# Performance work log

Measured on AMD Instinct MI355X. Metric: run time of the kernel, lower is better.

Reference implementation:

```python
import jax, jax.numpy as jnp
import numpy as np

B, CIN, H, W = 16, 15, 256, 256
C, L, M = 64, 4, 16
ENV, D1D = 40, 4
HEAD_IN = C + ENV + D1D
BN_EPS = 1e-5


def setup_inputs() -> dict:
    key = jax.random.key(0)
    ks = iter(jax.random.split(key, 40))
    nrm = lambda shape: jax.random.normal(next(ks), shape, dtype=jnp.float32)
    scale = (2.0 / (C + C)) ** 0.5
    uni = lambda shape: scale * (jax.random.uniform(next(ks), shape, dtype=jnp.float32) - 0.5)
    d = {
        'grid': nrm((B, CIN, H, W)),
        'env': nrm((B, ENV)),
        'd1d': nrm((B, D1D)),
        'lift_w': nrm((C, CIN)) * 0.1, 'lift_b': nrm((C,)) * 0.01,
        'w1r': uni((L, C, C, M, M)), 'w1i': uni((L, C, C, M, M)),
        'w2r': uni((L, C, C, M, M)), 'w2i': uni((L, C, C, M, M)),
        'skip_w': nrm((L, C, C)) * 0.1, 'skip_b': nrm((L, C)) * 0.01,
        'bn_g': jnp.ones((L, C)), 'bn_b': jnp.zeros((L, C)),
        'bn_m': nrm((L, C)) * 0.01, 'bn_v': jnp.abs(nrm((L, C))) * 0.1 + 1.0,
        'proj_w': nrm((C, C)) * 0.1, 'proj_b': nrm((C,)) * 0.01,
        'dw1': nrm((128, HEAD_IN)) * 0.05, 'db1': nrm((128,)) * 0.01,
        'dw2': nrm((64, 128)) * 0.05, 'db2': nrm((64,)) * 0.01,
        'dw3': nrm((8, 64)) * 0.05, 'db3': nrm((8,)) * 0.01,
        'iw1': nrm((128, HEAD_IN)) * 0.05, 'ib1': nrm((128,)) * 0.01,
        'iw2': nrm((64, 128)) * 0.05, 'ib2': nrm((64,)) * 0.01,
        'iw3': nrm((4, 64)) * 0.05, 'ib3': nrm((4,)) * 0.01,
    }
    return d


def _spectral(x, w1, w2):
    # x: [B,C,H,W] real; w1,w2: [C,C,M,M] complex
    h, w = x.shape[-2], x.shape[-1]
    xft = jnp.fft.rfft2(x)  # [B,C,H,W//2+1] complex
    top = jnp.einsum('bixy,ioxy->boxy', xft[:, :, :M, :M], w1)
    bot = jnp.einsum('bixy,ioxy->boxy', xft[:, :, -M:, :M], w2)
    out_ft = jnp.zeros(xft.shape, dtype=xft.dtype)
    out_ft = out_ft.at[:, :, :M, :M].set(top).at[:, :, h - M:, :M].set(bot)
    return jnp.fft.irfft2(out_ft, s=(h, w))


def _conv1x1(x, w, b):
    return jnp.einsum('bchw,oc->bohw', x, w) + b[None, :, None, None]


def _gelu(x):
    return jax.nn.gelu(x, approximate=False)


def reference(grid, env, d1d, lift_w, lift_b, w1r, w1i, w2r, w2i, skip_w, skip_b,
              bn_g, bn_b, bn_m, bn_v, proj_w, proj_b,
              dw1, db1, dw2, db2, dw3, db3, iw1, ib1, iw2, ib2, iw3, ib3):
    x = _gelu(_conv1x1(grid, lift_w, lift_b))
    for l in range(L):
        residual = x
        w1 = w1r[l] + 1j * w1i[l]
        w2 = w2r[l] + 1j * w2i[l]
        y = _spectral(x, w1, w2) + _conv1x1(x, skip_w[l], skip_b[l])
        # BatchNorm2d in eval mode (running stats), dropout is identity at eval
        y = (y - bn_m[l][None, :, None, None]) * jax.lax.rsqrt(bn_v[l] + BN_EPS)[None, :, None, None]
        y = y * bn_g[l][None, :, None, None] + bn_b[l][None, :, None, None]
        x = _gelu(y) + residual
    x = _gelu(_conv1x1(x, proj_w, proj_b))
    x = x.mean(axis=(-2, -1))  # [B,C]
    x = jnp.concatenate([x, env, d1d], axis=-1)  # [B, C+44]
    h = _gelu(x @ dw1.T + db1)
    h = _gelu(h @ dw2.T + db2)
    out_dir = h @ dw3.T + db3
    g = _gelu(x @ iw1.T + ib1)
    g = _gelu(g @ iw2.T + ib2)
    out_int = g @ iw3.T + ib3
    return out_dir, out_int
```

## Files before the change

### kernel.cpp

```cpp
#include <hip/hip_runtime.h>
#include <hip/hip_bf16.h>
#include <math.h>

#define B_ 16
#define CIN_ 15
#define C_ 64
#define L_ 4

typedef __attribute__((ext_vector_type(8))) short short8;
typedef __attribute__((ext_vector_type(4))) short short4v;
typedef __attribute__((ext_vector_type(4))) float f32x4;

__device__ __forceinline__ float gelu_f(float x) {
    float z = fabsf(x) * 0.70710678118654752440f;
    float t = __builtin_amdgcn_rcpf(fmaf(0.3275911f, z, 1.0f));
    float p = t * fmaf(t, fmaf(t, fmaf(t, fmaf(t, 1.061405429f, -1.453152027f), 1.421413741f), -0.284496736f), 0.254829592f);
    float e = __expf(-z * z);
    float E = fmaf(-p, e, 1.0f);
    return 0.5f * fmaf(fabsf(x), E, x);
}

__device__ __forceinline__ unsigned short f2bf(float x) {
    __hip_bfloat16 h = __float2bfloat16(x);
    return *(unsigned short*)&h;
}
__device__ __forceinline__ float bf2f(unsigned short u) {
    __hip_bfloat16 h = *(__hip_bfloat16*)&u;
    return __bfloat162float(h);
}
__device__ __forceinline__ f32x4 mfma16(short8 a, short8 b, f32x4 c) {
    return __builtin_amdgcn_mfma_f32_16x16x32_bf16(a, b, c, 0, 0, 0);
}

#define TWO_PI_OVER_256 0.024543692606170259674f

__global__ __launch_bounds__(256) void k_prep(const float* __restrict__ skip_w,
                                              const float* __restrict__ bn_g, const float* __restrict__ bn_v,
                                              const float* __restrict__ proj_w,
                                              unsigned short* __restrict__ TfH, unsigned short* __restrict__ TfL,
                                              unsigned short* __restrict__ TiH, unsigned short* __restrict__ TiL,
                                              unsigned short* __restrict__ WH, unsigned short* __restrict__ WL,
                                              unsigned short* __restrict__ PH, unsigned short* __restrict__ PL,
                                              unsigned short* __restrict__ FcH, unsigned short* __restrict__ FcL,
                                              unsigned short* __restrict__ FsH, unsigned short* __restrict__ FsL,
                                              unsigned short* __restrict__ FnH, unsigned short* __restrict__ FnL,
                                              unsigned short* __restrict__ IcH, unsigned short* __restrict__ IcL,
                                              unsigned short* __restrict__ IsH, unsigned short* __restrict__ IsL,
                                              unsigned short* __restrict__ InH, unsigned short* __restrict__ InL) {
    int id = blockIdx.x * 256 + threadIdx.x;
    if (id < 8192) {
        int col = id >> 8, w = id & 255;
        int kk = (col < 16) ? col : (col - 16);
        float s, c;
        sincosf(TWO_PI_OVER_256 * (float)((w * kk) & 255), &s, &c);
        float v = (col < 16) ? c : -s;
        unsigned short hi = f2bf(v);
        TfH[id] = hi; TfL[id] = f2bf(v - bf2f(hi));
    } else if (id < 16384) {
        int idx = id - 8192;
        int w = idx >> 5, k = idx & 31, ky = k >> 1;
        float s, c;
        sincosf(TWO_PI_OVER_256 * (float)((w * ky) & 255), &s, &c);
        float v = (k & 1) ? -s : c;
        unsigned short hi = f2bf(v);
        TiH[idx] = hi; TiL[idx] = f2bf(v - bf2f(hi));
    } else if (id < 32768) {
        int idx = id - 16384;
        int lco = idx >> 6;
        float scl = bn_g[lco] * rsqrtf(bn_v[lco] + 1e-5f);
        float v = scl * skip_w[idx];
        unsigned short hi = f2bf(v);
        WH[idx] = hi; WL[idx] = f2bf(v - bf2f(hi));
    } else if (id < 36864) {
        int idx = id - 32768;
        float v = proj_w[idx];
        unsigned short hi = f2bf(v);
        PH[idx] = hi; PL[idx] = f2bf(v - bf2f(hi));
    } else if (id < 45056) {
        int idx = id - 36864;
        int j = idx >> 8, h = idx & 255;
        int kxu = j + ((j < 16) ? 0 : 224);
        float s, c;
        sincosf(TWO_PI_OVER_256 * (float)((h * kxu) & 255), &s, &c);
        unsigned short ch = f2bf(c);
        FcH[idx] = ch; FcL[idx] = f2bf(c - bf2f(ch));
        unsigned short sh = f2bf(s);
        unsigned short sl = f2bf(s - bf2f(sh));
        FsH[idx] = sh; FsL[idx] = sl;
        FnH[idx] = sh ^ 0x8000; FnL[idx] = sl ^ 0x8000;
    } else if (id < 53248) {
        int idx = id - 45056;
        int h = idx >> 5, j = idx & 31;
        int kxu = j + ((j < 16) ? 0 : 224);
        float s, c;
        sincosf(TWO_PI_OVER_256 * (float)((h * kxu) & 255), &s, &c);
        unsigned short ch = f2bf(c);
        IcH[idx] = ch; IcL[idx] = f2bf(c - bf2f(ch));
        unsigned short sh = f2bf(s);
        unsigned short sl = f2bf(s - bf2f(sh));
        IsH[idx] = sh; IsL[idx] = sl;
        InH[idx] = sh ^ 0x8000; InL[idx] = sl ^ 0x8000;
    }
}

__global__ __launch_bounds__(256) void k_lift(const float* __restrict__ g, const float* __restrict__ lw,
                                              const float* __restrict__ lb, unsigned short* __restrict__ X,
                                              const unsigned short* __restrict__ TfH, const unsigned short* __restrict__ TfL,
                                              float2* __restrict__ Y) {
    __shared__ float gs[CIN_][256];
    __shared__ float lws[C_ * CIN_];
    __shared__ float lbs[C_];
    __shared__ unsigned short xl[64 * 264];
    int b = blockIdx.x >> 8, h = blockIdx.x & 255;
    int t = threadIdx.x;
    for (int ci = 0; ci < CIN_; ci++)
        gs[ci][t] = g[((b * CIN_ + ci) * 256 + h) * 256 + t];
    for (int idx = t; idx < C_ * CIN_; idx += 256) lws[idx] = lw[idx];
    if (t < C_) lbs[t] = lb[t];
    __syncthreads();
    for (int co = 0; co < C_; co++) {
        float acc = lbs[co];
        #pragma unroll
        for (int ci = 0; ci < CIN_; ci++) acc += gs[ci][t] * lws[co * CIN_ + ci];
        xl[co * 264 + t] = f2bf(gelu_f(acc));
    }
    __syncthreads();
    {
        int wv = t >> 6, ln = t & 63;
        int lx = ln & 15, q = ln >> 4;
        f32x4 fa0 = {0.f, 0.f, 0.f, 0.f}, fa1 = {0.f, 0.f, 0.f, 0.f};
        for (int ks = 0; ks < 8; ks++) {
            int k0 = ks * 32;
            short8 a = *(const short8*)(&xl[(wv * 16 + lx) * 264 + k0 + q * 8]);
            short8 bh0 = *(const short8*)(TfH + lx * 256 + k0 + q * 8);
            short8 bl0 = *(const short8*)(TfL + lx * 256 + k0 + q * 8);
            short8 bh1 = *(const short8*)(TfH + (16 + lx) * 256 + k0 + q * 8);
            short8 bl1 = *(const short8*)(TfL + (16 + lx) * 256 + k0 + q * 8);
            fa0 = mfma16(a, bh0, fa0); fa0 = mfma16(a, bl0, fa0);
            fa1 = mfma16(a, bh1, fa1); fa1 = mfma16(a, bl1, fa1);
        }
        #pragma unroll
        for (int r = 0; r < 4; r++) {
            int c = wv * 16 + q * 4 + r;
            Y[(b * 64 + c) * 4096 + h * 16 + lx] = make_float2(fa0[r], fa1[r]);
        }
    }
    unsigned short* Xg = X + (size_t)(b * 64) * 65536 + h * 256;
    #pragma unroll
    for (int r = 0; r < 8; r++) {
        int idx = r * 256 + t;
        int c = idx >> 5, w8 = idx & 31;
        *(short8*)(Xg + c * 65536 + w8 * 8) = *(const short8*)(&xl[c * 264 + w8 * 8]);
    }
}

__global__ __launch_bounds__(256) void k_fwd_h(const float2* __restrict__ Y, float2* __restrict__ XF,
                                               const unsigned short* __restrict__ FcH, const unsigned short* __restrict__ FcL,
                                               const unsigned short* __restrict__ FsH, const unsigned short* __restrict__ FsL,
                                               const unsigned short* __restrict__ FnH, const unsigned short* __restrict__ FnL) {
    __shared__ float red[4][2][2][64][4];
    int bc = blockIdx.x;
    int t = threadIdx.x;
    int wv = t >> 6, l = t & 63, lx = l & 15, g = l >> 4;
    const float2* Yb = Y + (size_t)bc * 4096;
    f32x4 aR[2], aI[2];
    aR[0] = (f32x4){0.f,0.f,0.f,0.f}; aR[1] = aR[0]; aI[0] = aR[0]; aI[1] = aR[0];
    #pragma unroll
    for (int kk = 0; kk < 2; kk++) {
        int ks = wv * 2 + kk;
        short8 yrh, yrl, yih, yil;
        #pragma unroll
        for (int j = 0; j < 8; j++) {
            float2 v = Yb[(ks * 32 + g * 8 + j) * 16 + lx];
            unsigned short h1 = f2bf(v.x);
            yrh[j] = (short)h1; yrl[j] = (short)f2bf(v.x - bf2f(h1));
            unsigned short h2 = f2bf(v.y);
            yih[j] = (short)h2; yil[j] = (short)f2bf(v.y - bf2f(h2));
        }
        #pragma unroll
        for (int rt = 0; rt < 2; rt++) {
            int base = (rt * 16 + lx) * 256 + ks * 32 + g * 8;
            short8 ch = *(const short8*)(FcH + base);
            short8 cl = *(const short8*)(FcL + base);
            short8 sh = *(const short8*)(FsH + base);
            short8 sl = *(const short8*)(FsL + base);
            short8 nh = *(const short8*)(FnH + base);
            short8 nl = *(const short8*)(FnL + base);
            aR[rt] = mfma16(ch, yrh, aR[rt]);
            aR[rt] = mfma16(ch, yrl, aR[rt]);
            aR[rt] = mfma16(cl, yrh, aR[rt]);
            aR[rt] = mfma16(sh, yih, aR[rt]);
            aR[rt] = mfma16(sh, yil, aR[rt]);
            aR[rt] = mfma16(sl, yih, aR[rt]);
            aI[rt] = mfma16(ch, yih, aI[rt]);
            aI[rt] = mfma16(ch, yil, aI[rt]);
            aI[rt] = mfma16(cl, yih, aI[rt]);
            aI[rt] = mfma16(nh, yrh, aI[rt]);
            aI[rt] = mfma16(nh, yrl, aI[rt]);
            aI[rt] = mfma16(nl, yrh, aI[rt]);
        }
    }
    #pragma unroll
    for (int rt = 0; rt < 2; rt++) {
        *(f32x4*)&red[wv][rt][0][l][0] = aR[rt];
        *(f32x4*)&red[wv][rt][1][l][0] = aI[rt];
    }
    __syncthreads();
    if (t < 128) {
        int rt = t >> 6, ll = t & 63;
        int llx = ll & 15, gg = ll >> 4;
        f32x4 R = *(const f32x4*)&red[0][rt][0][ll][0];
        f32x4 I = *(const f32x4*)&red[0][rt][1][ll][0];
        #pragma unroll
        for (int w = 1; w < 4; w++) {
            R += *(const f32x4*)&red[w][rt][0][ll][0];
            I += *(const f32x4*)&red[w][rt][1][ll][0];
        }
        #pragma unroll
        for (int r = 0; r < 4; r++) {
            int j = rt * 16 + gg * 4 + r;
            XF[(j * 16 + llx) * 1024 + bc] = make_float2(R[r], I[r]);
        }
    }
}

__global__ __launch_bounds__(256) void k_repack(const float* __restrict__ w1r, const float* __restrict__ w1i,
                                                const float* __restrict__ w2r, const float* __restrict__ w2i,
                                                float2* __restrict__ WPK, int l) {
    int j = blockIdx.x >> 6, i = blockIdx.x & 63;
    int t = threadIdx.x;
    int ky = t & 15, o0 = (t >> 4) * 4;
    int x = j & 15;
    const float* wr = (j < 16) ? w1r : w2r;
    const float* wi = (j < 16) ? w1i : w2i;
    size_t sb = ((size_t)(l * 64 + i) * 64 + o0) * 256 + x * 16 + ky;
    float r0 = wr[sb];       float v0 = wi[sb];
    float r1 = wr[sb + 256]; float v1 = wi[sb + 256];
    float r2 = wr[sb + 512]; float v2 = wi[sb + 512];
    float r3 = wr[sb + 768]; float v3 = wi[sb + 768];
    float4* dst = (float4*)(WPK + ((size_t)(j * 16 + ky) * 64 + i) * 64 + o0);
    dst[0] = make_float4(r0, v0, r1, v1);
    dst[1] = make_float4(r2, v2, r3, v3);
}

__global__ __launch_bounds__(256) void k_mix(const float2* __restrict__ XF, const float2* __restrict__ WPK,
                                             float2* __restrict__ YF) {
    __shared__ float2 xs[1024];
    __shared__ float2 wls[4096];
    int s = blockIdx.x;
    int t = threadIdx.x;
    for (int idx = t; idx < 1024; idx += 256) xs[idx] = XF[s * 1024 + idx];
    for (int idx = t; idx < 4096; idx += 256) wls[idx] = WPK[(size_t)s * 4096 + idx];
    __syncthreads();
    int o = t & 63, bg = t >> 6;
    float2 acc[4];
    #pragma unroll
    for (int q = 0; q < 4; q++) acc[q] = make_float2(0.f, 0.f);
    for (int i = 0; i < 64; i++) {
        float2 wv = wls[i * 64 + o];
        #pragma unroll
        for (int q = 0; q < 4; q++) {
            float2 xv = xs[(bg * 4 + q) * 64 + i];
            acc[q].x += xv.x * wv.x - xv.y * wv.y;
            acc[q].y += xv.x * wv.y + xv.y * wv.x;
        }
    }
    #pragma unroll
    for (int q = 0; q < 4; q++) {
        int b = bg * 4 + q;
        YF[(b * 64 + o) * 512 + s] = acc[q];
    }
}

__global__ __launch_bounds__(256) void k_inv_h(const float2* __restrict__ YF, float2* __restrict__ Z,
                                               const unsigned short* __restrict__ IcH, const unsigned short* __restrict__ IcL,
                                               const unsigned short* __restrict__ IsH, const unsigned short* __restrict__ IsL,
                                               const unsigned short* __restrict__ InH, const unsigned short* __restrict__ InL) {
    int bc = blockIdx.x;
    int t = threadIdx.x;
    int wv = t >> 6, l = t & 63, lx = l & 15, g = l >> 4;
    const float2* Yb = YF + (size_t)bc * 512;
    short8 xrh, xrl, xih, xil;
    #pragma unroll
    for (int jj = 0; jj < 8; jj++) {
        float2 v = Yb[(g * 8 + jj) * 16 + lx];
        unsigned short h1 = f2bf(v.x);
        xrh[jj] = (short)h1; xrl[jj] = (short)f2bf(v.x - bf2f(h1));
        unsigned short h2 = f2bf(v.y);
        xih[jj] = (short)h2; xil[jj] = (short)f2bf(v.y - bf2f(h2));
    }
    float2* Zb = Z + (size_t)bc * 4096;
    #pragma unroll
    for (int hh = 0; hh < 4; hh++) {
        int ht = wv * 4 + hh;
        int base = (ht * 16 + lx) * 32 + g * 8;
        short8 ch = *(const short8*)(IcH + base);
        short8 cl = *(const short8*)(IcL + base);
        short8 sh = *(const short8*)(IsH + base);
        short8 sl = *(const short8*)(IsL + base);
        short8 nh = *(const short8*)(InH + base);
        short8 nl = *(const short8*)(InL + base);
        f32x4 aR = {0.f,0.f,0.f,0.f}, aI = {0.f,0.f,0.f,0.f};
        aR = mfma16(ch, xrh, aR); aR = mfma16(ch, xrl, aR); aR = mfma16(cl, xrh, aR);
        aR = mfma16(nh, xih, aR); aR = mfma16(nh, xil, aR); aR = mfma16(nl, xih, aR);
        aI = mfma16(sh, xrh, aI); aI = mfma16(sh, xrl, aI); aI = mfma16(sl, xrh, aI);
        aI = mfma16(ch, xih, aI); aI = mfma16(ch, xil, aI); aI = mfma16(cl, xih, aI);
        #pragma unroll
        for (int r = 0; r < 4; r++) {
            int h = ht * 16 + g * 4 + r;
            Zb[h * 16 + lx] = make_float2(aR[r], aI[r]);
        }
    }
}

__global__ __launch_bounds__(256) void k_tail(unsigned short* __restrict__ X, const float2* __restrict__ Z,
                                              const unsigned short* __restrict__ WH, const unsigned short* __restrict__ WL,
                                              const float* __restrict__ sbl, const float* __restrict__ bng,
                                              const float* __restrict__ bnb, const float* __restrict__ bnm,
                                              const float* __restrict__ bnv,
                                              const unsigned short* __restrict__ TiH, const unsigned short* __restrict__ TiL,
                                              const unsigned short* __restrict__ TfH, const unsigned short* __restrict__ TfL,
                                              float2* __restrict__ Y, int mode,
                                              const unsigned short* __restrict__ PH, const unsigned short* __restrict__ PL,
                                              const float* __restrict__ pb, float* __restrict__ ACC) {
    __shared__ unsigned short xl[64 * 264];
    __shared__ float cbs[64];
    __shared__ float pacc[64];
    __shared__ float pbs[64];
    int b = blockIdx.x >> 8, h = blockIdx.x & 255;
    int t = threadIdx.x;
    unsigned short* Xg = X + (size_t)(b * 64) * 65536 + h * 256;
    #pragma unroll
    for (int r = 0; r < 8; r++) {
        int idx = r * 256 + t;
        int c = idx >> 5, w8 = idx & 31;
        *(short8*)(&xl[c * 264 + w8 * 8]) = *(const short8*)(Xg + c * 65536 + w8 * 8);
    }
    if (t < 64) {
        float scl = bng[t] * rsqrtf(bnv[t] + 1e-5f);
        cbs[t] = scl * (sbl[t] - bnm[t]) + bnb[t];
        pacc[t] = 0.f;
        pbs[t] = pb[t];
    }
    __syncthreads();

    int wv = t >> 6, ln = t & 63;
    int lx = ln & 15, q = ln >> 4;

    short8 azh[4], azl[4];
    {
        const float2* Zg = Z + (size_t)(b * 64) * 4096 + h * 16;
        #pragma unroll
        for (int mt = 0; mt < 4; mt++) {
            int co = mt * 16 + lx;
            float scl = bng[co] * rsqrtf(bnv[co] + 1e-5f);
            float f2v = scl * (2.0f / 65536.0f);
            float f0 = (q == 0) ? (scl * (1.0f / 65536.0f)) : f2v;
            const float4* zp = (const float4*)(Zg + (size_t)co * 4096 + q * 4);
            float4 z0 = zp[0], z1 = zp[1];
            float v[8];
            v[0] = z0.x * f0;  v[1] = z0.y * f0;
            v[2] = z0.z * f2v; v[3] = z0.w * f2v;
            v[4] = z1.x * f2v; v[5] = z1.y * f2v;
            v[6] = z1.z * f2v; v[7] = z1.w * f2v;
            #pragma unroll
            for (int j = 0; j < 8; j++) {
                unsigned short hv = f2bf(v[j]);
                azh[mt][j] = (short)hv;
                azl[mt][j] = (short)f2bf(v[j] - bf2f(hv));
            }
        }
    }

    #pragma unroll 1
    for (int nt = 0; nt < 4; nt++) {
        int w0 = wv * 64 + nt * 16;
        int w = w0 + lx;
        f32x4 acc[4];
        #pragma unroll
        for (int mt = 0; mt < 4; mt++) acc[mt] = (f32x4){0.f, 0.f, 0.f, 0.f};
        {
            short8 tah = *(const short8*)(TiH + w * 32 + q * 8);
            short8 tal = *(const short8*)(TiL + w * 32 + q * 8);
            #pragma unroll
            for (int mt = 0; mt < 4; mt++) {
                acc[mt] = mfma16(tah, azh[mt], acc[mt]);
                acc[mt] = mfma16(tah, azl[mt], acc[mt]);
                acc[mt] = mfma16(tal, azh[mt], acc[mt]);
            }
        }
        #pragma unroll
        for (int ks = 0; ks < 2; ks++) {
            int k0 = ks * 32;
            short8 afr;
            #pragma unroll
            for (int j = 0; j < 8; j++)
                afr[j] = (short)xl[(k0 + q * 8 + j) * 264 + w];
            #pragma unroll
            for (int mt = 0; mt < 4; mt++) {
                short8 bh = *(const short8*)(WH + (mt * 16 + lx) * 64 + k0 + q * 8);
                short8 bl = *(const short8*)(WL + (mt * 16 + lx) * 64 + k0 + q * 8);
                acc[mt] = mfma16(afr, bh, acc[mt]);
                acc[mt] = mfma16(afr, bl, acc[mt]);
            }
        }
        #pragma unroll
        for (int mt = 0; mt < 4; mt++) {
            int co = mt * 16 + lx;
            float cb = cbs[co];
            unsigned short* xp = &xl[co * 264 + w0 + q * 4];
            short4v old = *(const short4v*)xp;
            short4v nw;
            #pragma unroll
            for (int r = 0; r < 4; r++) {
                float y = acc[mt][r] + cb;
                float v = gelu_f(y) + bf2f((unsigned short)old[r]);
                nw[r] = (short)f2bf(v);
            }
            *(short4v*)xp = nw;
        }
    }
    __syncthreads();

    if (mode == 1) {
        f32x4 fa0 = {0.f, 0.f, 0.f, 0.f}, fa1 = {0.f, 0.f, 0.f, 0.f};
        for (int ks = 0; ks < 8; ks++) {
            int k0 = ks * 32;
            short8 a = *(const short8*)(&xl[(wv * 16 + lx) * 264 + k0 + q * 8]);
            short8 bh0 = *(const short8*)(TfH + lx * 256 + k0 + q * 8);
            short8 bl0 = *(const short8*)(TfL + lx * 256 + k0 + q * 8);
            short8 bh1 = *(const short8*)(TfH + (16 + lx) * 256 + k0 + q * 8);
            short8 bl1 = *(const short8*)(TfL + (16 + lx) * 256 + k0 + q * 8);
            fa0 = mfma16(a, bh0, fa0); fa0 = mfma16(a, bl0, fa0);
            fa1 = mfma16(a, bh1, fa1); fa1 = mfma16(a, bl1, fa1);
        }
        #pragma unroll
        for (int r = 0; r < 4; r++) {
            int c = wv * 16 + q * 4 + r;
            Y[(b * 64 + c) * 4096 + h * 16 + lx] = make_float2(fa0[r], fa1[r]);
        }
        #pragma unroll
        for (int r = 0; r < 8; r++) {
            int idx = r * 256 + t;
            int c = idx >> 5, w8 = idx & 31;
            *(short8*)(Xg + c * 65536 + w8 * 8) = *(const short8*)(&xl[c * 264 + w8 * 8]);
        }
    } else {
        float psum[4][4];
        #pragma unroll
        for (int mt = 0; mt < 4; mt++)
            #pragma unroll
            for (int r = 0; r < 4; r++) psum[mt][r] = 0.f;
        #pragma unroll 1
        for (int nt = 0; nt < 4; nt++) {
            int w = wv * 64 + nt * 16 + lx;
            f32x4 acc[4];
            #pragma unroll
            for (int mt = 0; mt < 4; mt++) acc[mt] = (f32x4){0.f, 0.f, 0.f, 0.f};
            #pragma unroll
            for (int ks = 0; ks < 2; ks++) {
                int k0 = ks * 32;
                short8 afr;
                #pragma unroll
                for (int j = 0; j < 8; j++)
                    afr[j] = (short)xl[(k0 + q * 8 + j) * 264 + w];
                #pragma unroll
                for (int mt = 0; mt < 4; mt++) {
                    short8 bh = *(const short8*)(PH + (mt * 16 + lx) * 64 + k0 + q * 8);
                    short8 bl = *(const short8*)(PL + (mt * 16 + lx) * 64 + k0 + q * 8);
                    acc[mt] = mfma16(afr, bh, acc[mt]);
                    acc[mt] = mfma16(afr, bl, acc[mt]);
                }
            }
            #pragma unroll
            for (int mt = 0; mt < 4; mt++) {
                int co = mt * 16 + lx;
                #pragma unroll
                for (int r = 0; r < 4; r++)
                    psum[mt][r] += gelu_f(acc[mt][r] + pbs[co]);
            }
        }
        #pragma unroll
        for (int mt = 0; mt < 4; mt++) {
            int co = mt * 16 + lx;
            float s = psum[mt][0] + psum[mt][1] + psum[mt][2] + psum[mt][3];
            s += __shfl_xor(s, 16, 64);
            s += __shfl_xor(s, 32, 64);
            if (q == 0) atomicAdd(&pacc[co], s);
        }
        __syncthreads();
        if (t < 64) atomicAdd(&ACC[b * 64 + t], pacc[t]);
    }
}

__global__ __launch_bounds__(128) void k_head(const float* __restrict__ ACC, const float* __restrict__ env,
                                              const float* __restrict__ d1d,
                                              const float* __restrict__ dw1, const float* __restrict__ db1,
                                              const float* __restrict__ dw2, const float* __restrict__ db2,
                                              const float* __restrict__ dw3, const float* __restrict__ db3,
                                              const float* __restrict__ iw1, const float* __restrict__ ib1,
                                              const float* __restrict__ iw2, const float* __restrict__ ib2,
                                              const float* __restrict__ iw3, const float* __restrict__ ib3,
                                              float* __restrict__ out) {
    __shared__ float xc[108];
    __shared__ float h1[128];
    __shared__ float h2[64];
    int b = blockIdx.x, t = threadIdx.x;
    if (t < 64) xc[t] = ACC[b * 64 + t] * (1.0f / 65536.0f);
    else if (t < 104) xc[t] = env[b * 40 + (t - 64)];
    else if (t < 108) xc[t] = d1d[b * 4 + (t - 104)];
    __syncthreads();
    {
        float a = db1[t];
        for (int k = 0; k < 108; k++) a += xc[k] * dw1[t * 108 + k];
        h1[t] = gelu_f(a);
    }
    __syncthreads();
    if (t < 64) {
        float a = db2[t];
        for (int k = 0; k < 128; k++) a += h1[k] * dw2[t * 128 + k];
        h2[t] = gelu_f(a);
    }
    __syncthreads();
    if (t < 8) {
        float a = db3[t];
        for (int k = 0; k < 64; k++) a += h2[k] * dw3[t * 64 + k];
        out[b * 8 + t] = a;
    }
    __syncthreads();
    {
        float a = ib1[t];
        for (int k = 0; k < 108; k++) a += xc[k] * iw1[t * 108 + k];
        h1[t] = gelu_f(a);
    }
    __syncthreads();
    if (t < 64) {
        float a = ib2[t];
        for (int k = 0; k < 128; k++) a += h1[k] * iw2[t * 128 + k];
        h2[t] = gelu_f(a);
    }
    __syncthreads();
    if (t < 4) {
        float a = ib3[t];
        for (int k = 0; k < 64; k++) a += h2[k] * iw3[t * 64 + k];
        out[128 + b * 4 + t] = a;
    }
}

extern "C" void kernel_launch(void* const* d_in, const int* in_sizes, int n_in,
                              void* d_out, int out_size, void* d_ws, size_t ws_size,
                              hipStream_t stream) {
    const float* grid_  = (const float*)d_in[0];
    const float* env    = (const float*)d_in[1];
    const float* d1d    = (const float*)d_in[2];
    const float* lift_w = (const float*)d_in[3];
    const float* lift_b = (const float*)d_in[4];
    const float* w1r    = (const float*)d_in[5];
    const float* w1i    = (const float*)d_in[6];
    const float* w2r    = (const float*)d_in[7];
    const float* w2i    = (const float*)d_in[8];
    const float* skip_w = (const float*)d_in[9];
    const float* skip_b = (const float*)d_in[10];
    const float* bn_g   = (const float*)d_in[11];
    const float* bn_b   = (const float*)d_in[12];
    const float* bn_m   = (const float*)d_in[13];
    const float* bn_v   = (const float*)d_in[14];
    const float* proj_w = (const float*)d_in[15];
    const float* proj_b = (const float*)d_in[16];
    const float* dw1 = (const float*)d_in[17];
    const float* db1 = (const float*)d_in[18];
    const float* dw2 = (const float*)d_in[19];
    const float* db2 = (const float*)d_in[20];
    const float* dw3 = (const float*)d_in[21];
    const float* db3 = (const float*)d_in[22];
    const float* iw1 = (const float*)d_in[23];
    const float* ib1 = (const float*)d_in[24];
    const float* iw2 = (const float*)d_in[25];
    const float* ib2 = (const float*)d_in[26];
    const float* iw3 = (const float*)d_in[27];
    const float* ib3 = (const float*)d_in[28];

    char* ws = (char*)d_ws;
    unsigned short* X   = (unsigned short*)(ws);
    float2* S   = (float2*)(ws + 134217728);
    float2* XF  = (float2*)(ws + 167772160);
    float2* YF  = (float2*)(ws + 171966464);
    float2* WPK = (float2*)(ws + 176160768);
    float*  ACC = (float*)(ws + 192937984);
    unsigned short* TfH = (unsigned short*)(ws + 192942080);
    unsigned short* TfL = (unsigned short*)(ws + 192958464);
    unsigned short* TiH = (unsigned short*)(ws + 192974848);
    unsigned short* TiL = (unsigned short*)(ws + 192991232);
    unsigned short* WH  = (unsigned short*)(ws + 193007616);
    unsigned short* WL  = (unsigned short*)(ws + 193040384);
    unsigned short* PH  = (unsigned short*)(ws + 193073152);
    unsigned short* PL  = (unsigned short*)(ws + 193081344);
    unsigned short* FcH = (unsigned short*)(ws + 193089536);
    unsigned short* FcL = (unsigned short*)(ws + 193105920);
    unsigned short* FsH = (unsigned short*)(ws + 193122304);
    unsigned short* FsL = (unsigned short*)(ws + 193138688);
    unsigned short* FnH = (unsigned short*)(ws + 193155072);
    unsigned short* FnL = (unsigned short*)(ws + 193171456);
    unsigned short* IcH = (unsigned short*)(ws + 193187840);
    unsigned short* IcL = (unsigned short*)(ws + 193204224);
    unsigned short* IsH = (unsigned short*)(ws + 193220608);
    unsigned short* IsL = (unsigned short*)(ws + 193236992);
    unsigned short* InH = (unsigned short*)(ws + 193253376);
    unsigned short* InL = (unsigned short*)(ws + 193269760);

    hipMemsetAsync(ACC, 0, 1024 * sizeof(float), stream);
    k_prep<<<208, 256, 0, stream>>>(skip_w, bn_g, bn_v, proj_w, TfH, TfL, TiH, TiL, WH, WL, PH, PL,
                                    FcH, FcL, FsH, FsL, FnH, FnL, IcH, IcL, IsH, IsL, InH, InL);
    k_lift<<<4096, 256, 0, stream>>>(grid_, lift_w, lift_b, X, TfH, TfL, S);
    for (int l = 0; l < L_; l++) {
        k_repack<<<2048, 256, 0, stream>>>(w1r, w1i, w2r, w2i, WPK, l);
        k_fwd_h<<<1024, 256, 0, stream>>>(S, XF, FcH, FcL, FsH, FsL, FnH, FnL);
        k_mix<<<512, 256, 0, stream>>>(XF, WPK, YF);
        k_inv_h<<<1024, 256, 0, stream>>>(YF, S, IcH, IcL, IsH, IsL, InH, InL);
        k_tail<<<4096, 256, 0, stream>>>(X, S, WH + l * 4096, WL + l * 4096,
                                         skip_b + l * 64, bn_g + l * 64, bn_b + l * 64,
                                         bn_m + l * 64, bn_v + l * 64,
                                         TiH, TiL, TfH, TfL, S, (l < 3) ? 1 : 2,
                                         PH, PL, proj_b, ACC);
    }
    k_head<<<16, 128, 0, stream>>>(ACC, env, d1d, dw1, db1, dw2, db2, dw3, db3,
                                   iw1, ib1, iw2, ib2, iw3, ib3, (float*)d_out);
}
```

Before: 1.128 ms.

## Fuse spectral weight repack into mix kernel and prefetch twiddle fragments in tail

Removes the separate per-layer repack kernel: k_mix now gathers the real and imaginary weight planes straight from the original layout into shared memory. This saves one launch and a write plus re-read of the packed buffer in each layer, at the cost of strided, poorly coalesced global reads (stride 256 floats) inside k_mix. Separately, the tail kernel software-prefetches the next iteration's TiH/TiL fragments before issuing the current MFMAs, to hide load latency.

New measurement: 1.165 ms. 1.03x slower.

```diff
diff --git a/kernel.cpp b/kernel.cpp
--- a/kernel.cpp
+++ b/kernel.cpp
@@ -224,33 +224,23 @@
     }
 }
 
-__global__ __launch_bounds__(256) void k_repack(const float* __restrict__ w1r, const float* __restrict__ w1i,
-                                                const float* __restrict__ w2r, const float* __restrict__ w2i,
-                                                float2* __restrict__ WPK, int l) {
-    int j = blockIdx.x >> 6, i = blockIdx.x & 63;
-    int t = threadIdx.x;
-    int ky = t & 15, o0 = (t >> 4) * 4;
-    int x = j & 15;
-    const float* wr = (j < 16) ? w1r : w2r;
-    const float* wi = (j < 16) ? w1i : w2i;
-    size_t sb = ((size_t)(l * 64 + i) * 64 + o0) * 256 + x * 16 + ky;
-    float r0 = wr[sb];       float v0 = wi[sb];
-    float r1 = wr[sb + 256]; float v1 = wi[sb + 256];
-    float r2 = wr[sb + 512]; float v2 = wi[sb + 512];
-    float r3 = wr[sb + 768]; float v3 = wi[sb + 768];
-    float4* dst = (float4*)(WPK + ((size_t)(j * 16 + ky) * 64 + i) * 64 + o0);
-    dst[0] = make_float4(r0, v0, r1, v1);
-    dst[1] = make_float4(r2, v2, r3, v3);
-}
-
-__global__ __launch_bounds__(256) void k_mix(const float2* __restrict__ XF, const float2* __restrict__ WPK,
-                                             float2* __restrict__ YF) {
+__global__ __launch_bounds__(256) void k_mix(const float2* __restrict__ XF,
+                                             const float* __restrict__ w1r, const float* __restrict__ w1i,
+                                             const float* __restrict__ w2r, const float* __restrict__ w2i,
+                                             float2* __restrict__ YF, int l) {
     __shared__ float2 xs[1024];
     __shared__ float2 wls[4096];
     int s = blockIdx.x;
     int t = threadIdx.x;
+    int j = s >> 4, ky = s & 15, x = j & 15;
+    const float* wr = (j < 16) ? w1r : w2r;
+    const float* wi = (j < 16) ? w1i : w2i;
     for (int idx = t; idx < 1024; idx += 256) xs[idx] = XF[s * 1024 + idx];
-    for (int idx = t; idx < 4096; idx += 256) wls[idx] = WPK[(size_t)s * 4096 + idx];
+    for (int idx = t; idx < 4096; idx += 256) {
+        int i = idx >> 6, o = idx & 63;
+        size_t src = ((size_t)(l * 64 + i) * 64 + o) * 256 + x * 16 + ky;
+        wls[idx] = make_float2(wr[src], wi[src]);
+    }
     __syncthreads();
     int o = t & 63, bg = t >> 6;
     float2 acc[4];
@@ -372,22 +362,25 @@
         }
     }
 
+    short8 tah = *(const short8*)(TiH + (wv * 64 + lx) * 32 + q * 8);
+    short8 tal = *(const short8*)(TiL + (wv * 64 + lx) * 32 + q * 8);
     #pragma unroll 1
     for (int nt = 0; nt < 4; nt++) {
         int w0 = wv * 64 + nt * 16;
         int w = w0 + lx;
+        short8 tah_c = tah, tal_c = tal;
+        if (nt < 3) {
+            tah = *(const short8*)(TiH + (w + 16) * 32 + q * 8);
+            tal = *(const short8*)(TiL + (w + 16) * 32 + q * 8);
+        }
         f32x4 acc[4];
         #pragma unroll
         for (int mt = 0; mt < 4; mt++) acc[mt] = (f32x4){0.f, 0.f, 0.f, 0.f};
-        {
-            short8 tah = *(const short8*)(TiH + w * 32 + q * 8);
-            short8 tal = *(const short8*)(TiL + w * 32 + q * 8);
-            #pragma unroll
-            for (int mt = 0; mt < 4; mt++) {
-                acc[mt] = mfma16(tah, azh[mt], acc[mt]);
-                acc[mt] = mfma16(tah, azl[mt], acc[mt]);
-                acc[mt] = mfma16(tal, azh[mt], acc[mt]);
-            }
+        #pragma unroll
+        for (int mt = 0; mt < 4; mt++) {
+            acc[mt] = mfma16(tah_c, azh[mt], acc[mt]);
+            acc[mt] = mfma16(tah_c, azl[mt], acc[mt]);
+            acc[mt] = mfma16(tal_c, azh[mt], acc[mt]);
         }
         #pragma unroll
         for (int ks = 0; ks < 2; ks++) {
@@ -585,7 +578,6 @@
     float2* S   = (float2*)(ws + 134217728);
     float2* XF  = (float2*)(ws + 167772160);
     float2* YF  = (float2*)(ws + 171966464);
-    float2* WPK = (float2*)(ws + 176160768);
     float*  ACC = (float*)(ws + 192937984);
     unsigned short* TfH = (unsigned short*)(ws + 192942080);
     unsigned short* TfL = (unsigned short*)(ws + 192958464);
@@ -613,9 +605,8 @@
                                     FcH, FcL, FsH, FsL, FnH, FnL, IcH, IcL, IsH, IsL, InH, InL);
     k_lift<<<4096, 256, 0, stream>>>(grid_, lift_w, lift_b, X, TfH, TfL, S);
     for (int l = 0; l < L_; l++) {
-        k_repack<<<2048, 256, 0, stream>>>(w1r, w1i, w2r, w2i, WPK, l);
         k_fwd_h<<<1024, 256, 0, stream>>>(S, XF, FcH, FcL, FsH, FsL, FnH, FnL);
-        k_mix<<<512, 256, 0, stream>>>(XF, WPK, YF);
+        k_mix<<<512, 256, 0, stream>>>(XF, w1r, w1i, w2r, w2i, YF, l);
         k_inv_h<<<1024, 256, 0, stream>>>(YF, S, IcH, IcL, IsH, IsL, InH, InL);
         k_tail<<<4096, 256, 0, stream>>>(X, S, WH + l * 4096, WL + l * 4096,
                                          skip_b + l * 64, bn_g + l * 64, bn_b + l * 64,
```
